# Kernel optimization log

Measured on AMD Instinct MI355X. Metric: run time of the kernel, lower is better.

## Reference

```python
import jax, jax.numpy as jnp
import numpy as np

B, L, D, H, DH = 2, 2048, 1024, 16, 64
THETA_T = 100.0
EPS_COS = 1e-6
EPS_NORM = 1e-6


def make_rope_tables(n_heads=H, d_head=DH, theta_t=THETA_T):
    dr = d_head // 12                      # 5 rotary freqs per head per axis
    n = n_heads * dr
    log_min, log_max = np.log(np.pi), np.log(10.0 * np.pi)
    f = np.exp(np.linspace(log_min, log_max, n + 1)[:-1])
    freqs = np.stack([f, f]).reshape(2, dr, n_heads).transpose(0, 2, 1)   # (2, H, dr)
    t_freqs = (theta_t ** (-np.arange(n, dtype=np.float64) / n)).reshape(dr, n_heads).T  # (H, dr)
    return jnp.asarray(freqs, jnp.float32), jnp.asarray(t_freqs, jnp.float32)


def rms_norm(x, scale, eps=EPS_NORM):
    ms = jnp.mean(x.astype(jnp.float32) ** 2, axis=-1, keepdims=True)
    return x * (scale.astype(jnp.float32) * jax.lax.rsqrt(ms + eps)).astype(x.dtype)


def rope_theta(pos, pos_orig, time, freqs, t_freqs):
    # pos_to_use: (b, l, c=2, xy=2), mapped to [-1, 1]
    pos_use = jnp.stack([pos_orig, pos], axis=2) * 2.0 - 1.0
    theta_w = pos_use[..., 0][:, :, :, None, None] * freqs[0]      # b l 2 H dr
    theta_h = pos_use[..., 1][:, :, :, None, None] * freqs[1]      # b l 2 H dr
    theta_t = time[:, :, None, None, None] * t_freqs               # b l 1 H dr
    theta = jnp.concatenate([theta_h, theta_w, theta_t], axis=2)   # b l 5 H dr
    b, l = theta.shape[0], theta.shape[1]
    theta = jnp.transpose(theta, (0, 1, 3, 2, 4)).reshape(b, l, H, -1)  # b l H (5*dr)
    return theta


def apply_rotary_emb(x, theta):
    d = theta.shape[-1]
    x1, x2, x3 = x[..., :d], x[..., d:2 * d], x[..., 2 * d:]
    cos, sin = jnp.cos(theta), jnp.sin(theta)
    y1 = x1 * cos - x2 * sin
    y2 = x2 * cos + x1 * sin
    return jnp.concatenate([y1, y2, x3], axis=-1)


def scale_for_cosine_sim(q, k, scale, eps=EPS_COS):
    sq = jnp.sum(q * q, axis=-1, keepdims=True)
    sk = jnp.sum(k * k, axis=-1, keepdims=True)
    sqrt_scale = jnp.sqrt(scale)                         # (H,1,1) -> broadcasts to (b,H,l,1)
    return q * (sqrt_scale * jax.lax.rsqrt(sq + eps)), k * (sqrt_scale * jax.lax.rsqrt(sk + eps))


def setup_inputs() -> dict:
    key = jax.random.key(0)
    ks = jax.random.split(key, 8)
    return {
        "x": jax.random.normal(ks[0], (B, L, D), jnp.float32),
        "pos": jax.random.uniform(ks[1], (B, L, 2), jnp.float32),
        "pos_orig": jax.random.uniform(ks[2], (B, L, 2), jnp.float32),
        "time": jax.random.uniform(ks[3], (B, L), jnp.float32),
        "w_qkv": jax.random.normal(ks[4], (3 * D, D), jnp.float32) * (D ** -0.5),
        "w_out": jax.random.normal(ks[5], (D, D), jnp.float32) * (D ** -0.5),
        "w_up": jax.random.normal(ks[6], (4 * D, D), jnp.float32) * (D ** -0.5),
        "w_down": jax.random.normal(ks[7], (D, 4 * D), jnp.float32) * ((4 * D) ** -0.5),
        "norm1_scale": jnp.ones((D,), jnp.float32),
        "norm2_scale": jnp.ones((D,), jnp.float32),
        "qk_scale": jnp.full((H, 1, 1), 10.0, jnp.float32),
    }


def reference(x, pos, pos_orig, time, w_qkv, w_out, w_up, w_down,
              norm1_scale, norm2_scale, qk_scale):
    freqs, t_freqs = make_rope_tables()
    b, l, _ = x.shape

    # --- attention block (pre-norm) ---
    xn = rms_norm(x, norm1_scale)
    qkv = jnp.einsum('bld,ed->ble', xn, w_qkv)                  # b l 3D
    q, k, v = jnp.split(qkv, 3, axis=-1)
    q = q.reshape(b, l, H, DH)
    k = k.reshape(b, l, H, DH)
    v = v.reshape(b, l, H, DH).transpose(0, 2, 1, 3)            # b H l dh

    theta = rope_theta(pos, pos_orig, time, freqs, t_freqs)      # b l H 25
    q = apply_rotary_emb(q, theta).transpose(0, 2, 1, 3)         # b H l dh
    k = apply_rotary_emb(k, theta).transpose(0, 2, 1, 3)

    q, k = scale_for_cosine_sim(q, k, qk_scale)                  # cosine-sim QK norm
    scores = jnp.einsum('bhqd,bhkd->bhqk', q, k)                 # scale=1 (already folded in)
    probs = jax.nn.softmax(scores, axis=-1)
    attn = jnp.einsum('bhqk,bhkd->bhqd', probs, v)
    attn = attn.transpose(0, 2, 1, 3).reshape(b, l, D)
    x = x + jnp.einsum('bld,ed->ble', attn, w_out)

    h = rms_norm(x, norm2_scale)
    h = jax.nn.gelu(jnp.einsum('bld,ed->ble', h, w_up), approximate=True)
    x = x + jnp.einsum('ble,de->bld', h, w_down)
    return x
```

## Files before the change

kernel.cpp:

```cpp
#include <hip/hip_runtime.h>

#define B_ 2
#define L_ 2048
#define D_ 1024
#define H_ 16
#define DH_ 64

typedef float f32x4 __attribute__((ext_vector_type(4)));
typedef __bf16 bf16x8 __attribute__((ext_vector_type(8)));

__device__ __forceinline__ ushort f2bf(float f) {
  unsigned u = __float_as_uint(f);
  u += 0x7fffu + ((u >> 16) & 1u);
  return (ushort)(u >> 16);
}
__device__ __forceinline__ float bf2f(ushort h) {
  return __uint_as_float(((unsigned)h) << 16);
}

__device__ __forceinline__ void gload_lds16(const void* g, void* l) {
  __builtin_amdgcn_global_load_lds(
      (const __attribute__((address_space(1))) unsigned*)g,
      (__attribute__((address_space(3))) unsigned*)l, 16, 0, 0);
}

__global__ __launch_bounds__(256) void cast_all_kernel(const float* __restrict__ w0,
                                                       const float* __restrict__ w1,
                                                       const float* __restrict__ w2,
                                                       const float* __restrict__ w3,
                                                       ushort* __restrict__ o0,
                                                       ushort* __restrict__ o1,
                                                       ushort* __restrict__ o2,
                                                       ushort* __restrict__ o3) {
  int i = blockIdx.x * 256 + threadIdx.x;
  const float* src;
  ushort* dst;
  int j = i;
  if (j < 786432) { src = w0; dst = o0; }
  else if (j < 786432 + 262144) { j -= 786432; src = w1; dst = o1; }
  else if (j < 786432 + 262144 + 1048576) { j -= 786432 + 262144; src = w2; dst = o2; }
  else { j -= 786432 + 262144 + 1048576; src = w3; dst = o3; }
  float4 v = ((const float4*)src)[j];
  ushort4 o;
  o.x = f2bf(v.x); o.y = f2bf(v.y); o.z = f2bf(v.z); o.w = f2bf(v.w);
  ((ushort4*)dst)[j] = o;
}

template <typename T>
__global__ __launch_bounds__(256) void rmsnorm_kernel(const T* __restrict__ x,
                                                      const float* __restrict__ scale,
                                                      ushort* __restrict__ out) {
  int row = blockIdx.x, t = threadIdx.x;
  float4 v;
  if constexpr (sizeof(T) == 4) {
    v = ((const float4*)((const float*)x + (size_t)row * D_))[t];
  } else {
    ushort4 u = ((const ushort4*)((const ushort*)x + (size_t)row * D_))[t];
    v.x = bf2f(u.x); v.y = bf2f(u.y); v.z = bf2f(u.z); v.w = bf2f(u.w);
  }
  float ss = v.x * v.x + v.y * v.y + v.z * v.z + v.w * v.w;
#pragma unroll
  for (int d = 1; d < 64; d <<= 1) ss += __shfl_xor(ss, d);
  __shared__ float wsum[4];
  if ((t & 63) == 0) wsum[t >> 6] = ss;
  __syncthreads();
  float tot = wsum[0] + wsum[1] + wsum[2] + wsum[3];
  float r = rsqrtf(tot * (1.0f / D_) + 1e-6f);
  float4 sc = ((const float4*)scale)[t];
  ushort4 o;
  o.x = f2bf(v.x * sc.x * r); o.y = f2bf(v.y * sc.y * r);
  o.z = f2bf(v.z * sc.z * r); o.w = f2bf(v.w * sc.w * r);
  ((ushort4*)(out + (size_t)row * D_))[t] = o;
}

template <int EPI, int BM, int BN, int DEPTH, int XR, int XC, bool CTFAST>
__global__ __launch_bounds__(256) void gemm_nt(const ushort* __restrict__ A,
                                               const ushort* __restrict__ Bw,
                                               void* __restrict__ Cout,
                                               const void* __restrict__ resid,
                                               int M, int N, int K, int Klen) {
  constexpr int WROWS = BM / 2, WCOLS = BN / 2;
  constexpr int MR = WROWS / 16, NR = WCOLS / 16;
  constexpr int ALOADS = BM / 64, BLOADS = BN / 64;
  constexpr int NLOADS = ALOADS + BLOADS;
  __shared__ __align__(16) ushort Als[DEPTH][BM * 32];
  __shared__ __align__(16) ushort Bls[DEPTH][BN * 32];
  const int tid = threadIdx.x;
  const int lane = tid & 63;
  const int w = tid >> 6;
  const int wr = w >> 1, wc = w & 1;
  const int bid = blockIdx.y * gridDim.x + blockIdx.x;
  const int xcd = bid & 7;
  const int i0 = bid >> 3;
  const int CR = gridDim.x / XR, CC = gridDim.y / XC;
  int rt, ct;
  if constexpr (CTFAST) {
    rt = (xcd % XR) * CR + (i0 / CC);
    ct = (xcd / XR) * CC + (i0 % CC);
  } else {
    rt = (xcd % XR) * CR + (i0 % CR);
    ct = (xcd / XR) * CC + (i0 / CR);
  }
  const int row0 = rt * BM;
  const int col0 = ct * BN;
  const int koff = blockIdx.z * Klen;
  const ushort* Ab = A + (size_t)row0 * K + koff;
  const ushort* Bb = Bw + (size_t)col0 * K + koff;
  const int sr = tid >> 2;
  const int scA = (((tid & 3) ^ ((tid >> 3) & 3)) * 8);
  const int fr = lane & 15;
  const int fg = lane >> 4;
  f32x4 zero = {0.f, 0.f, 0.f, 0.f};
  f32x4 acc[MR][NR];
#pragma unroll
  for (int m = 0; m < MR; m++)
#pragma unroll
    for (int n = 0; n < NR; n++) acc[m][n] = zero;

  auto stage = [&](int slot, int kt) {
#pragma unroll
    for (int i2 = 0; i2 < ALOADS; i2++)
      gload_lds16(Ab + (size_t)(sr + 64 * i2) * K + kt + scA, &Als[slot][i2 * 2048 + tid * 8]);
#pragma unroll
    for (int i2 = 0; i2 < BLOADS; i2++)
      gload_lds16(Bb + (size_t)(sr + 64 * i2) * K + kt + scA, &Bls[slot][i2 * 2048 + tid * 8]);
  };
  const int nt = Klen >> 5;
#pragma unroll
  for (int p = 0; p < DEPTH - 1; p++) stage(p, p << 5);
  int cur = 0, sbuf = DEPTH - 1;
  for (int t = 0; t < nt; t++) {
    const int ahead = nt - 1 - t;
    if constexpr (DEPTH == 3) {
      if (ahead >= 1) asm volatile("s_waitcnt vmcnt(%0)" ::"i"(NLOADS) : "memory");
      else            asm volatile("s_waitcnt vmcnt(0)" ::: "memory");
    } else if constexpr (DEPTH == 4) {
      if (ahead >= 2)      asm volatile("s_waitcnt vmcnt(%0)" ::"i"(2 * NLOADS) : "memory");
      else if (ahead == 1) asm volatile("s_waitcnt vmcnt(%0)" ::"i"(NLOADS) : "memory");
      else                 asm volatile("s_waitcnt vmcnt(0)" ::: "memory");
    } else {
      if (ahead >= 3)      asm volatile("s_waitcnt vmcnt(%0)" ::"i"(3 * NLOADS) : "memory");
      else if (ahead == 2) asm volatile("s_waitcnt vmcnt(%0)" ::"i"(2 * NLOADS) : "memory");
      else if (ahead == 1) asm volatile("s_waitcnt vmcnt(%0)" ::"i"(NLOADS) : "memory");
      else                 asm volatile("s_waitcnt vmcnt(0)" ::: "memory");
    }
    __builtin_amdgcn_s_barrier();
    __builtin_amdgcn_sched_barrier(0);
    if (t + DEPTH - 1 < nt) {
      stage(sbuf, (t + DEPTH - 1) << 5);
      sbuf = (sbuf == DEPTH - 1) ? 0 : sbuf + 1;
    }
    bf16x8 af[MR], bfr[NR];
#pragma unroll
    for (int m = 0; m < MR; m++) {
      int rA = wr * WROWS + m * 16 + fr;
      af[m] = *(const bf16x8*)&Als[cur][rA * 32 + ((fg ^ ((rA >> 1) & 3)) << 3)];
    }
#pragma unroll
    for (int n = 0; n < NR; n++) {
      int rB = wc * WCOLS + n * 16 + fr;
      bfr[n] = *(const bf16x8*)&Bls[cur][rB * 32 + ((fg ^ ((rB >> 1) & 3)) << 3)];
    }
    __builtin_amdgcn_s_setprio(1);
#pragma unroll
    for (int m = 0; m < MR; m++)
#pragma unroll
      for (int n = 0; n < NR; n++)
        acc[m][n] = __builtin_amdgcn_mfma_f32_16x16x32_bf16(af[m], bfr[n], acc[m][n], 0, 0, 0);
    __builtin_amdgcn_s_setprio(0);
    cur = (cur == DEPTH - 1) ? 0 : cur + 1;
  }
  const int orow = row0 + wr * WROWS + fg * 4;
  const int ocol = col0 + wc * WCOLS + fr;
  float* Pz = (float*)Cout + (size_t)blockIdx.z * M * N;
#pragma unroll
  for (int m = 0; m < MR; m++) {
#pragma unroll
    for (int j = 0; j < 4; j++) {
      int r = orow + m * 16 + j;
#pragma unroll
      for (int n = 0; n < NR; n++) {
        int cidx = ocol + n * 16;
        size_t idx = (size_t)r * N + cidx;
        float v = acc[m][n][j];
        if (EPI == 0) {
          ((ushort*)Cout)[idx] = f2bf(v);
        } else if (EPI == 1) {
          ((ushort*)Cout)[idx] = f2bf(((const float*)resid)[idx] + v);
        } else if (EPI == 2) {
          float g = 0.5f * v * (1.0f + tanhf(0.7978845608f * (v + 0.044715f * v * v * v)));
          ((ushort*)Cout)[idx] = f2bf(g);
        } else if (EPI == 3) {
          ((float*)Cout)[idx] = bf2f(((const ushort*)resid)[idx]) + v;
        } else {
          Pz[idx] = v;
        }
      }
    }
  }
}

__global__ __launch_bounds__(256) void reduce_down_kernel(const float* __restrict__ P0,
                                                          const float* __restrict__ P1,
                                                          const ushort* __restrict__ residb,
                                                          float* __restrict__ out) {
  int i = blockIdx.x * 256 + threadIdx.x;
  float4 a = ((const float4*)P0)[i];
  float4 b = ((const float4*)P1)[i];
  ushort4 r = ((const ushort4*)residb)[i];
  float4 o;
  o.x = a.x + b.x + bf2f(r.x);
  o.y = a.y + b.y + bf2f(r.y);
  o.z = a.z + b.z + bf2f(r.z);
  o.w = a.w + b.w + bf2f(r.w);
  ((float4*)out)[i] = o;
}

__global__ __launch_bounds__(256) void rope_kernel(const ushort* __restrict__ qkv,
                                                   const float* __restrict__ pos,
                                                   const float* __restrict__ pos_orig,
                                                   const float* __restrict__ timep,
                                                   const float* __restrict__ qk_scale,
                                                   ushort* __restrict__ qr,
                                                   ushort* __restrict__ kr) {
  int gw = (blockIdx.x * 256 + threadIdx.x) >> 6;
  int lane = threadIdx.x & 63;
  int h = gw & 15;
  int row = gw >> 4;
  int b = row >> 11;
  int l = row & (L_ - 1);
  float qv = bf2f(qkv[(size_t)row * 3072 + h * 64 + lane]);
  float kv = bf2f(qkv[(size_t)row * 3072 + 1024 + h * 64 + lane]);
  float c = 1.0f, s = 0.0f;
  if (lane < 50) {
    int idx = lane < 25 ? lane : lane - 25;
    int sg = idx / 5, d = idx % 5;
    int fi = d * 16 + h;
    float th;
    if (sg == 4) {
      th = timep[row] * __expf(-(float)fi * 0.05756462732485115f);
    } else {
      float fr = 3.14159265358979323846f * __expf((float)fi * 0.028782313662425575f);
      const float* psrc = (sg == 0 || sg == 2) ? pos_orig : pos;
      int comp = (sg < 2) ? 1 : 0;
      th = (2.0f * psrc[(size_t)row * 2 + comp] - 1.0f) * fr;
    }
    s = sinf(th);
    c = cosf(th);
  }
  int partner = lane < 25 ? lane + 25 : lane - 25;
  float qp = __shfl(qv, partner, 64);
  float kp = __shfl(kv, partner, 64);
  float yq, yk;
  if (lane < 25) { yq = qv * c - qp * s; yk = kv * c - kp * s; }
  else if (lane < 50) { yq = qv * c + qp * s; yk = kv * c + kp * s; }
  else { yq = qv; yk = kv; }
  float sq = yq * yq, sk = yk * yk;
#pragma unroll
  for (int d = 1; d < 64; d <<= 1) { sq += __shfl_xor(sq, d); sk += __shfl_xor(sk, d); }
  float scl = sqrtf(qk_scale[h]);
  float qo = yq * scl * rsqrtf(sq + 1e-6f);
  float ko = yk * scl * rsqrtf(sk + 1e-6f);
  size_t o = ((size_t)(b * 16 + h) * L_ + l) * 64 + lane;
  qr[o] = f2bf(qo);
  kr[o] = f2bf(ko);
}

__global__ __launch_bounds__(256) void vtrans_kernel(const ushort* __restrict__ qkv,
                                                     ushort* __restrict__ vT) {
  __shared__ __align__(16) ushort tile[64][72];
  int t = threadIdx.x;
  int lt = blockIdx.x;
  int bh = blockIdx.y;
  int b = bh >> 4, h = bh & 15;
  int r = t >> 3, c0 = (t & 7) * 8;
#pragma unroll
  for (int half = 0; half < 2; half++) {
    const ushort* src =
        qkv + (size_t)(b * L_ + lt * 64 + r + half * 32) * 3072 + 2048 + h * 64 + c0;
    *(uint4*)&tile[r + half * 32][c0] = *(const uint4*)src;
  }
  __syncthreads();
#pragma unroll
  for (int half = 0; half < 2; half++) {
    int dh = r + half * 32;
    unsigned p0 = (unsigned)tile[c0 + 0][dh] | ((unsigned)tile[c0 + 1][dh] << 16);
    unsigned p1 = (unsigned)tile[c0 + 2][dh] | ((unsigned)tile[c0 + 3][dh] << 16);
    unsigned p2 = (unsigned)tile[c0 + 4][dh] | ((unsigned)tile[c0 + 5][dh] << 16);
    unsigned p3 = (unsigned)tile[c0 + 6][dh] | ((unsigned)tile[c0 + 7][dh] << 16);
    uint4 o; o.x = p0; o.y = p1; o.z = p2; o.w = p3;
    *(uint4*)&vT[((size_t)bh * 64 + dh) * L_ + lt * 64 + c0] = o;
  }
}

__global__ __launch_bounds__(256) void attn_kernel(const ushort* __restrict__ qr,
                                                   const ushort* __restrict__ kr,
                                                   const ushort* __restrict__ vT,
                                                   ushort* __restrict__ attnb) {
  __shared__ __align__(16) ushort Kls[2][64 * 64];
  __shared__ __align__(16) ushort Vls[2][64 * 64];
  __shared__ __align__(16) ushort Pls[4][16 * 64];
  const int tid = threadIdx.x, lane = tid & 63, w = tid >> 6;
  const int bid = blockIdx.x;
  const int qp = (bid >> 3) & 15;
  const int bh = (bid & 7) | ((bid >> 7) << 3);
  const int b = bh >> 4;
  const int fr = lane & 15, fg = lane >> 4;
  const ushort* Qb0 = qr + ((size_t)bh * L_ + qp * 128 + w * 16) * 64;
  const ushort* Qb1 = Qb0 + 64 * 64;
  bf16x8 qf0[2], qf1[2];
#pragma unroll
  for (int c = 0; c < 2; c++) {
    qf0[c] = *(const bf16x8*)(Qb0 + fr * 64 + c * 32 + fg * 8);
    qf1[c] = *(const bf16x8*)(Qb1 + fr * 64 + c * 32 + fg * 8);
  }
  const ushort ob[8] = {0x3F80, 0x3F80, 0x3F80, 0x3F80, 0x3F80, 0x3F80, 0x3F80, 0x3F80};
  const bf16x8 ones = *(const bf16x8*)ob;
  f32x4 zero = {0.f, 0.f, 0.f, 0.f};
  f32x4 accO0[4], accO1[4], acc1_0 = zero, acc1_1 = zero;
#pragma unroll
  for (int n = 0; n < 4; n++) { accO0[n] = zero; accO1[n] = zero; }
  const int sr = tid >> 3;
  const int scz = (((tid & 7) ^ (sr & 7)) * 8);
  auto stage = [&](int buf, int kt) {
    gload_lds16(kr + ((size_t)bh * L_ + kt + sr) * 64 + scz, &Kls[buf][tid * 8]);
    gload_lds16(kr + ((size_t)bh * L_ + kt + 32 + sr) * 64 + scz, &Kls[buf][2048 + tid * 8]);
    gload_lds16(vT + ((size_t)bh * 64 + sr) * L_ + kt + scz, &Vls[buf][tid * 8]);
    gload_lds16(vT + ((size_t)bh * 64 + 32 + sr) * L_ + kt + scz, &Vls[buf][2048 + tid * 8]);
  };
  stage(0, 0);
  int cur = 0;
  for (int t = 0; t < (L_ >> 6); t++) {
    asm volatile("s_waitcnt vmcnt(0)" ::: "memory");
    __builtin_amdgcn_s_barrier();
    __builtin_amdgcn_sched_barrier(0);
    if (t + 1 < (L_ >> 6)) stage(cur ^ 1, (t + 1) << 6);
#pragma unroll
    for (int qs = 0; qs < 2; qs++) {
      const bf16x8* qf = qs ? qf1 : qf0;
      f32x4* accO = qs ? accO1 : accO0;
      f32x4& acc1 = qs ? acc1_1 : acc1_0;
      f32x4 sv[4];
#pragma unroll
      for (int n = 0; n < 4; n++) sv[n] = zero;
      __builtin_amdgcn_s_setprio(1);
#pragma unroll
      for (int c = 0; c < 2; c++) {
#pragma unroll
        for (int n = 0; n < 4; n++) {
          bf16x8 kf =
              *(const bf16x8*)&Kls[cur][(n * 16 + fr) * 64 + (((c * 4 + fg) ^ (fr & 7)) << 3)];
          sv[n] = __builtin_amdgcn_mfma_f32_16x16x32_bf16(qf[c], kf, sv[n], 0, 0, 0);
        }
      }
      __builtin_amdgcn_s_setprio(0);
#pragma unroll
      for (int j = 0; j < 4; j++) {
        int row = fg * 4 + j;
        int rbase = row * 64;
        int rx = row & 7;
#pragma unroll
        for (int n = 0; n < 4; n++) {
          float p = __builtin_amdgcn_exp2f(
              fmaf(sv[n][j], 1.4426950408889634f, -17.31234049066756f));
          int chunk = 2 * n + (fr >> 3);
          Pls[w][rbase + ((chunk ^ rx) << 3) + (fr & 7)] =
              (ushort)(__float_as_uint(p) >> 16);
        }
      }
      __builtin_amdgcn_s_setprio(1);
#pragma unroll
      for (int c = 0; c < 2; c++) {
        bf16x8 pa = *(const bf16x8*)&Pls[w][fr * 64 + (((c * 4 + fg) ^ (fr & 7)) << 3)];
#pragma unroll
        for (int n = 0; n < 4; n++) {
          bf16x8 vb =
              *(const bf16x8*)&Vls[cur][(n * 16 + fr) * 64 + (((c * 4 + fg) ^ (fr & 7)) << 3)];
          accO[n] = __builtin_amdgcn_mfma_f32_16x16x32_bf16(pa, vb, accO[n], 0, 0, 0);
        }
        acc1 = __builtin_amdgcn_mfma_f32_16x16x32_bf16(pa, ones, acc1, 0, 0, 0);
      }
      __builtin_amdgcn_s_setprio(0);
    }
    cur ^= 1;
  }
#pragma unroll
  for (int qs = 0; qs < 2; qs++) {
    const f32x4* accO = qs ? accO1 : accO0;
    const f32x4& acc1 = qs ? acc1_1 : acc1_0;
    float inv[4];
#pragma unroll
    for (int j = 0; j < 4; j++) inv[j] = 1.0f / acc1[j];
#pragma unroll
    for (int n = 0; n < 4; n++) {
#pragma unroll
      for (int j = 0; j < 4; j++) {
        float o = accO[n][j] * inv[j];
        int qrow = qp * 128 + qs * 64 + w * 16 + fg * 4 + j;
        int dh = fr + n * 16;
        attnb[(size_t)(b * L_ + qrow) * 1024 + (bh & 15) * 64 + dh] = f2bf(o);
      }
    }
  }
}

extern "C" void kernel_launch(void* const* d_in, const int* in_sizes, int n_in,
                              void* d_out, int out_size, void* d_ws, size_t ws_size,
                              hipStream_t stream) {
  const float* x = (const float*)d_in[0];
  const float* pos = (const float*)d_in[1];
  const float* pos_orig = (const float*)d_in[2];
  const float* timep = (const float*)d_in[3];
  const float* w_qkv = (const float*)d_in[4];
  const float* w_out = (const float*)d_in[5];
  const float* w_up = (const float*)d_in[6];
  const float* w_down = (const float*)d_in[7];
  const float* norm1 = (const float*)d_in[8];
  const float* norm2 = (const float*)d_in[9];
  const float* qk_scale = (const float*)d_in[10];
  float* out = (float*)d_out;
  char* ws = (char*)d_ws;
  size_t off = 0;
  auto alloc = [&](size_t bytes) {
    void* p = ws + off;
    off += bytes;
    return p;
  };
  ushort* xn = (ushort*)alloc(8ull << 20);
  ushort* qkvb = (ushort*)alloc(32ull << 20);
  ushort* qrb = (ushort*)alloc(8ull << 20);
  ushort* krb = (ushort*)alloc(8ull << 20);
  ushort* vTb = (ushort*)alloc(8ull << 20);
  ushort* attnb = (ushort*)alloc(8ull << 20);
  ushort* x1b = (ushort*)alloc(8ull << 20);
  ushort* wqkvb = (ushort*)alloc(6ull << 20);
  ushort* woutb = (ushort*)alloc(2ull << 20);
  ushort* wupb = (ushort*)alloc(8ull << 20);
  ushort* wdownb = (ushort*)alloc(8ull << 20);
  float* Ppart = (float*)qrb;

  cast_all_kernel<<<12288, 256, 0, stream>>>(w_qkv, w_out, w_up, w_down,
                                             wqkvb, woutb, wupb, wdownb);

  rmsnorm_kernel<float><<<4096, 256, 0, stream>>>(x, norm1, xn);
  gemm_nt<0, 128, 128, 3, 4, 2, false><<<dim3(32, 24), 256, 0, stream>>>(
      xn, wqkvb, qkvb, nullptr, 4096, 3072, 1024, 1024);
  rope_kernel<<<16384, 256, 0, stream>>>(qkvb, pos, pos_orig, timep, qk_scale, qrb, krb);
  vtrans_kernel<<<dim3(32, 32), 256, 0, stream>>>(qkvb, vTb);
  attn_kernel<<<512, 256, 0, stream>>>(qrb, krb, vTb, attnb);
  gemm_nt<1, 64, 64, 5, 4, 2, false><<<dim3(64, 16), 256, 0, stream>>>(
      attnb, woutb, x1b, x, 4096, 1024, 1024, 1024);
  rmsnorm_kernel<ushort><<<4096, 256, 0, stream>>>(x1b, norm2, xn);
  gemm_nt<2, 128, 128, 3, 4, 2, false><<<dim3(32, 32), 256, 0, stream>>>(
      xn, wupb, qkvb, nullptr, 4096, 4096, 1024, 1024);
  gemm_nt<4, 128, 128, 4, 4, 2, true><<<dim3(32, 8, 2), 256, 0, stream>>>(
      qkvb, wdownb, Ppart, nullptr, 4096, 1024, 4096, 2048);
  reduce_down_kernel<<<4096, 256, 0, stream>>>(Ppart, Ppart + (4u << 20), x1b, out);
}
```

Baseline: 284.3 us.

## Add 256x256-tile 8-wave GEMM with quadrant ping-pong for QKV and up projections

Adds a new gemm256 kernel that uses 512-thread blocks and 256x256 output tiles with K-step 64. It splits each tile into four quadrants, interleaving LDS fragment loads, next-tile global-to-LDS staging and MFMA bursts behind barriers and raised priority. The QKV and MLP-up GEMMs now use this kernel, which cuts global traffic per FLOP and overlaps loads with compute. The old gemm_nt loses its sched_barrier and setprio hints, which changes scheduling for the remaining out and down GEMMs. The big tile gives only 192/256 blocks on a 256-CU part, so occupancy and wave-tail effects are a risk.

Result: faster. 270.2 us (-5.0%).

```diff
diff --git a/kernel.cpp b/kernel.cpp
--- a/kernel.cpp
+++ b/kernel.cpp
@@ -22,6 +22,10 @@
   __builtin_amdgcn_global_load_lds(
       (const __attribute__((address_space(1))) unsigned*)g,
       (__attribute__((address_space(3))) unsigned*)l, 16, 0, 0);
+}
+
+__device__ __forceinline__ float gelu_f(float v) {
+  return 0.5f * v * (1.0f + tanhf(0.7978845608f * (v + 0.044715f * v * v * v)));
 }
 
 __global__ __launch_bounds__(256) void cast_all_kernel(const float* __restrict__ w0,
@@ -71,6 +75,173 @@
   o.x = f2bf(v.x * sc.x * r); o.y = f2bf(v.y * sc.y * r);
   o.z = f2bf(v.z * sc.z * r); o.w = f2bf(v.w * sc.w * r);
   ((ushort4*)(out + (size_t)row * D_))[t] = o;
+}
+
+template <int EPI, int XR, int XC>
+__global__ __launch_bounds__(512, 2) void gemm256(const ushort* __restrict__ A,
+                                                  const ushort* __restrict__ Bw,
+                                                  void* __restrict__ Cout,
+                                                  int M, int N, int K) {
+  __shared__ __align__(16) ushort Als[2][2][128 * 64];
+  __shared__ __align__(16) ushort Bls[2][2][128 * 64];
+  const int tid = threadIdx.x;
+  const int lane = tid & 63;
+  const int w = tid >> 6;
+  const int wm = w >> 2, wn = w & 3;
+  const int fr = lane & 15, fg = lane >> 4;
+  const int bid = blockIdx.y * gridDim.x + blockIdx.x;
+  const int xcd = bid & 7, i0 = bid >> 3;
+  const int CR = gridDim.x / XR, CC = gridDim.y / XC;
+  const int rt = (xcd % XR) * CR + (i0 % CR);
+  const int ct = (xcd / XR) * CC + (i0 / CR);
+  const int row0 = rt * 256, col0 = ct * 256;
+  const ushort* Ab = A + (size_t)row0 * K;
+  const ushort* Bb = Bw + (size_t)col0 * K;
+  const int srow = tid >> 3;
+  const int sxor = ((tid & 7) ^ (srow & 7)) * 8;
+
+  f32x4 acc[8][4];
+  f32x4 zero = {0.f, 0.f, 0.f, 0.f};
+#pragma unroll
+  for (int m = 0; m < 8; m++)
+#pragma unroll
+    for (int n = 0; n < 4; n++) acc[m][n] = zero;
+
+  auto stageA = [&](int buf, int half, int kt) {
+#pragma unroll
+    for (int i = 0; i < 2; i++)
+      gload_lds16(Ab + (size_t)(half * 128 + i * 64 + srow) * K + kt + sxor,
+                  &Als[buf][half][i * 4096 + tid * 8]);
+  };
+  auto stageB = [&](int buf, int half, int kt) {
+#pragma unroll
+    for (int i = 0; i < 2; i++)
+      gload_lds16(Bb + (size_t)(half * 128 + i * 64 + srow) * K + kt + sxor,
+                  &Bls[buf][half][i * 4096 + tid * 8]);
+  };
+  const int nt = K >> 6;
+  stageA(0, 0, 0); stageB(0, 0, 0); stageB(0, 1, 0); stageA(0, 1, 0);
+  asm volatile("s_waitcnt vmcnt(0)" ::: "memory");
+  __builtin_amdgcn_s_barrier();
+
+  bf16x8 afr[4][2], b0[2][2], b1[2][2];
+  for (int t = 0; t < nt; t++) {
+    const int cur = t & 1, nxt = cur ^ 1;
+    const int kn = (t + 1) << 6;
+    const bool more = (t + 1 < nt);
+#pragma unroll
+    for (int mf = 0; mf < 4; mf++)
+#pragma unroll
+      for (int ks = 0; ks < 2; ks++) {
+        int r = wm * 64 + mf * 16 + fr;
+        afr[mf][ks] = *(const bf16x8*)&Als[cur][0][r * 64 + (((ks * 4 + fg) ^ (r & 7)) << 3)];
+      }
+#pragma unroll
+    for (int nf = 0; nf < 2; nf++)
+#pragma unroll
+      for (int ks = 0; ks < 2; ks++) {
+        int c = wn * 32 + nf * 16 + fr;
+        b0[nf][ks] = *(const bf16x8*)&Bls[cur][0][c * 64 + (((ks * 4 + fg) ^ (c & 7)) << 3)];
+      }
+    if (more) stageA(nxt, 0, kn);
+    asm volatile("s_waitcnt vmcnt(4)" ::: "memory");
+    __builtin_amdgcn_s_barrier();
+    asm volatile("s_waitcnt lgkmcnt(0)" ::: "memory");
+    __builtin_amdgcn_sched_barrier(0);
+    __builtin_amdgcn_s_setprio(1);
+#pragma unroll
+    for (int mf = 0; mf < 4; mf++)
+#pragma unroll
+      for (int nf = 0; nf < 2; nf++)
+#pragma unroll
+        for (int ks = 0; ks < 2; ks++)
+          acc[mf][nf] =
+              __builtin_amdgcn_mfma_f32_16x16x32_bf16(afr[mf][ks], b0[nf][ks], acc[mf][nf], 0, 0, 0);
+    __builtin_amdgcn_s_setprio(0);
+    __builtin_amdgcn_s_barrier();
+#pragma unroll
+    for (int nf = 0; nf < 2; nf++)
+#pragma unroll
+      for (int ks = 0; ks < 2; ks++) {
+        int c = wn * 32 + nf * 16 + fr;
+        b1[nf][ks] = *(const bf16x8*)&Bls[cur][1][c * 64 + (((ks * 4 + fg) ^ (c & 7)) << 3)];
+      }
+    if (more) stageB(nxt, 0, kn);
+    asm volatile("s_waitcnt vmcnt(4)" ::: "memory");
+    __builtin_amdgcn_s_barrier();
+    asm volatile("s_waitcnt lgkmcnt(0)" ::: "memory");
+    __builtin_amdgcn_sched_barrier(0);
+    __builtin_amdgcn_s_setprio(1);
+#pragma unroll
+    for (int mf = 0; mf < 4; mf++)
+#pragma unroll
+      for (int nf = 0; nf < 2; nf++)
+#pragma unroll
+        for (int ks = 0; ks < 2; ks++)
+          acc[mf][2 + nf] =
+              __builtin_amdgcn_mfma_f32_16x16x32_bf16(afr[mf][ks], b1[nf][ks], acc[mf][2 + nf], 0, 0, 0);
+    __builtin_amdgcn_s_setprio(0);
+    __builtin_amdgcn_s_barrier();
+#pragma unroll
+    for (int mf = 0; mf < 4; mf++)
+#pragma unroll
+      for (int ks = 0; ks < 2; ks++) {
+        int r = wm * 64 + mf * 16 + fr;
+        afr[mf][ks] = *(const bf16x8*)&Als[cur][1][r * 64 + (((ks * 4 + fg) ^ (r & 7)) << 3)];
+      }
+    if (more) stageB(nxt, 1, kn);
+    asm volatile("s_waitcnt vmcnt(4)" ::: "memory");
+    __builtin_amdgcn_s_barrier();
+    asm volatile("s_waitcnt lgkmcnt(0)" ::: "memory");
+    __builtin_amdgcn_sched_barrier(0);
+    __builtin_amdgcn_s_setprio(1);
+#pragma unroll
+    for (int mf = 0; mf < 4; mf++)
+#pragma unroll
+      for (int nf = 0; nf < 2; nf++)
+#pragma unroll
+        for (int ks = 0; ks < 2; ks++)
+          acc[4 + mf][2 + nf] =
+              __builtin_amdgcn_mfma_f32_16x16x32_bf16(afr[mf][ks], b1[nf][ks], acc[4 + mf][2 + nf], 0, 0, 0);
+    __builtin_amdgcn_s_setprio(0);
+    __builtin_amdgcn_s_barrier();
+    if (more) stageA(nxt, 1, kn);
+    asm volatile("s_waitcnt vmcnt(4)" ::: "memory");
+    __builtin_amdgcn_s_barrier();
+    asm volatile("s_waitcnt lgkmcnt(0)" ::: "memory");
+    __builtin_amdgcn_sched_barrier(0);
+    __builtin_amdgcn_s_setprio(1);
+#pragma unroll
+    for (int mf = 0; mf < 4; mf++)
+#pragma unroll
+      for (int nf = 0; nf < 2; nf++)
+#pragma unroll
+        for (int ks = 0; ks < 2; ks++)
+          acc[4 + mf][nf] =
+              __builtin_amdgcn_mfma_f32_16x16x32_bf16(afr[mf][ks], b0[nf][ks], acc[4 + mf][nf], 0, 0, 0);
+    __builtin_amdgcn_s_setprio(0);
+    __builtin_amdgcn_s_barrier();
+  }
+  const int orow = row0 + wm * 64 + fg * 4;
+  const int ocol = col0 + wn * 32 + fr;
+#pragma unroll
+  for (int am = 0; am < 8; am++) {
+#pragma unroll
+    for (int j = 0; j < 4; j++) {
+      int r = orow + (am >> 2) * 128 + (am & 3) * 16 + j;
+#pragma unroll
+      for (int an = 0; an < 4; an++) {
+        int cidx = ocol + (an >> 1) * 128 + (an & 1) * 16;
+        size_t idx = (size_t)r * N + cidx;
+        float v = acc[am][an][j];
+        if (EPI == 0) {
+          ((ushort*)Cout)[idx] = f2bf(v);
+        } else {
+          ((ushort*)Cout)[idx] = f2bf(gelu_f(v));
+        }
+      }
+    }
+  }
 }
 
 template <int EPI, int BM, int BN, int DEPTH, int XR, int XC, bool CTFAST>
@@ -145,7 +316,6 @@
       else                 asm volatile("s_waitcnt vmcnt(0)" ::: "memory");
     }
     __builtin_amdgcn_s_barrier();
-    __builtin_amdgcn_sched_barrier(0);
     if (t + DEPTH - 1 < nt) {
       stage(sbuf, (t + DEPTH - 1) << 5);
       sbuf = (sbuf == DEPTH - 1) ? 0 : sbuf + 1;
@@ -161,13 +331,11 @@
       int rB = wc * WCOLS + n * 16 + fr;
       bfr[n] = *(const bf16x8*)&Bls[cur][rB * 32 + ((fg ^ ((rB >> 1) & 3)) << 3)];
     }
-    __builtin_amdgcn_s_setprio(1);
 #pragma unroll
     for (int m = 0; m < MR; m++)
 #pragma unroll
       for (int n = 0; n < NR; n++)
         acc[m][n] = __builtin_amdgcn_mfma_f32_16x16x32_bf16(af[m], bfr[n], acc[m][n], 0, 0, 0);
-    __builtin_amdgcn_s_setprio(0);
     cur = (cur == DEPTH - 1) ? 0 : cur + 1;
   }
   const int orow = row0 + wr * WROWS + fg * 4;
@@ -188,8 +356,7 @@
         } else if (EPI == 1) {
           ((ushort*)Cout)[idx] = f2bf(((const float*)resid)[idx] + v);
         } else if (EPI == 2) {
-          float g = 0.5f * v * (1.0f + tanhf(0.7978845608f * (v + 0.044715f * v * v * v)));
-          ((ushort*)Cout)[idx] = f2bf(g);
+          ((ushort*)Cout)[idx] = f2bf(gelu_f(v));
         } else if (EPI == 3) {
           ((float*)Cout)[idx] = bf2f(((const ushort*)resid)[idx]) + v;
         } else {
@@ -443,16 +610,14 @@
                                              wqkvb, woutb, wupb, wdownb);
 
   rmsnorm_kernel<float><<<4096, 256, 0, stream>>>(x, norm1, xn);
-  gemm_nt<0, 128, 128, 3, 4, 2, false><<<dim3(32, 24), 256, 0, stream>>>(
-      xn, wqkvb, qkvb, nullptr, 4096, 3072, 1024, 1024);
+  gemm256<0, 4, 2><<<dim3(16, 12), 512, 0, stream>>>(xn, wqkvb, qkvb, 4096, 3072, 1024);
   rope_kernel<<<16384, 256, 0, stream>>>(qkvb, pos, pos_orig, timep, qk_scale, qrb, krb);
   vtrans_kernel<<<dim3(32, 32), 256, 0, stream>>>(qkvb, vTb);
   attn_kernel<<<512, 256, 0, stream>>>(qrb, krb, vTb, attnb);
   gemm_nt<1, 64, 64, 5, 4, 2, false><<<dim3(64, 16), 256, 0, stream>>>(
       attnb, woutb, x1b, x, 4096, 1024, 1024, 1024);
   rmsnorm_kernel<ushort><<<4096, 256, 0, stream>>>(x1b, norm2, xn);
-  gemm_nt<2, 128, 128, 3, 4, 2, false><<<dim3(32, 32), 256, 0, stream>>>(
-      xn, wupb, qkvb, nullptr, 4096, 4096, 1024, 1024);
+  gemm256<2, 4, 2><<<dim3(16, 16), 512, 0, stream>>>(xn, wupb, qkvb, 4096, 4096, 1024);
   gemm_nt<4, 128, 128, 4, 4, 2, true><<<dim3(32, 8, 2), 256, 0, stream>>>(
       qkvb, wdownb, Ppart, nullptr, 4096, 1024, 4096, 2048);
   reduce_down_kernel<<<4096, 256, 0, stream>>>(Ppart, Ppart + (4u << 20), x1b, out);
```
